# Performance work log

Hardware: AMD Instinct MI355X
Metric: run time of the kernel (lower is better)

The kernel has to match this reference:

```python
import jax, jax.numpy as jnp
import numpy as np

B, T, D = 16, 512, 256          # batch, seq_len, d_model (= num features = num graph nodes N)
H, MC, K, DE, DH = 4, 4, 3, 10, 128
GS, SS, AS = 4, 6, 4            # global/sector/asset regime states
TAU = 0.5
STEPS = 3                       # diffusion steps
HID = max(64, D)
DEC_H = max(64, D // 2)


def setup_inputs() -> dict:
    key = jax.random.key(0)
    ks = iter(jax.random.split(key, 64))

    def nrm(shape, s=0.02):
        return (s * jax.random.normal(next(ks), shape)).astype(jnp.float32)

    z = lambda *s: jnp.zeros(s, jnp.float32)
    o = lambda *s: jnp.ones(s, jnp.float32)
    p = dict(
        x=jax.random.normal(next(ks), (B, T, D), dtype=jnp.float32),
        # hierarchical regime controller
        gW1=nrm((D, HID)), gb1=z(HID), g_ln_w=o(HID), g_ln_b=z(HID),
        gW2=nrm((HID, GS)), gb2=z(GS),
        sW1=nrm((D, HID)), sb1=z(HID), sW2=nrm((HID, D * SS)), sb2=z(D * SS),
        aW1=nrm((D, HID)), ab1=z(HID), aW2=nrm((HID, D * AS)), ab2=z(D * AS),
        global_prior=z(GS), sector_prior=z(SS), asset_prior=z(AS),
        g2f=nrm((GS, D)),
        sector_emb=jax.random.normal(next(ks), (SS, D), dtype=jnp.float32),
        asset_emb=jax.random.normal(next(ks), (AS, D), dtype=jnp.float32),
        # bidirectional temporal scan (BI-Mamba stand-in)
        decay_f=nrm((D,), 1.0), decay_b=nrm((D,), 1.0),
        tW=nrm((D, D)), tb=z(D),
        # Bayesian MAGAC + diffusion graph prior
        psi=nrm((H, D, DE), 0.1), log_sigma=jnp.full((H,), -2.0, jnp.float32),
        step_logits=jnp.linspace(-1.0, 0.5, STEPS).astype(jnp.float32),
        noise_scale=jnp.full((STEPS,), 0.05, jnp.float32),
        Wk=nrm((K + 1, T, DH)),
        mean_w=nrm((DH,)), mean_b=z(), lv_w=nrm((DH,)), lv_b=z(),
        # risk-aware decoder
        dW1=nrm((D, DEC_H)), db1=z(DEC_H), d_ln_w=o(DEC_H), d_ln_b=z(DEC_H),
        mW=nrm((DEC_H,)), mb=z(), lvW=nrm((DEC_H,)), lvb=z(),
        cW=nrm((DEC_H,)), cb=z(),
    )
    return p


def _ln(h, w, b):
    m = h.mean(-1, keepdims=True)
    v = h.var(-1, keepdims=True)  # biased, matches torch LayerNorm
    return (h - m) / jnp.sqrt(v + 1e-5) * w + b


def _gelu(h):
    return jax.nn.gelu(h, approximate=False)


def _gumbel_softmax(k, logits):
    u = jax.random.uniform(k, logits.shape, minval=1e-6, maxval=1.0 - 1e-6)
    g = -jnp.log(-jnp.log(u))
    return jax.nn.softmax((logits + g) / TAU, axis=-1)


def _fwd(x, gW1, gb1, g_ln_w, g_ln_b, gW2, gb2, sW1, sb1, sW2, sb2,
         aW1, ab1, aW2, ab2, global_prior, sector_prior, asset_prior,
         g2f, sector_emb, asset_emb, decay_f, decay_b, tW, tb,
         psi, log_sigma, step_logits, noise_scale, Wk,
         mean_w, mean_b, lv_w, lv_b,
         dW1, db1, d_ln_w, d_ln_b, mW, mb, lvW, lvb, cW, cb):
    rk = jax.random.key(42)
    k_g, k_s, k_a, k_eps, k_diff = jax.random.split(rk, 5)

    # ---- hierarchical regime controller ----
    seq_mean = x.mean(1)                               # (B, D)
    diff_summary = (x[:, 1:] - x[:, :-1]).mean(1)      # (B, D)
    g_logits = _gelu(_ln(seq_mean @ gW1 + gb1, g_ln_w, g_ln_b)) @ gW2 + gb2
    s_logits = (_gelu(seq_mean @ sW1 + sb1) @ sW2 + sb2).reshape(B, D, SS)
    a_logits = (_gelu(diff_summary @ aW1 + ab1) @ aW2 + ab2).reshape(B, D, AS)
    g_probs = _gumbel_softmax(k_g, g_logits)
    s_probs = _gumbel_softmax(k_s, s_logits)
    a_probs = _gumbel_softmax(k_a, a_logits)
    global_gate = g_probs @ g2f                                   # (B, D)
    # diagonal of einsum('bfs,sd->bfd') == einsum('bfs,sf->bf')
    sector_gate = jnp.einsum('bfs,sf->bf', s_probs, sector_emb)
    asset_gate = jnp.einsum('bfs,sf->bf', a_probs, asset_emb)
    feature_gate = jax.nn.sigmoid(global_gate + sector_gate + asset_gate)
    gated_x = x * feature_gate[:, None, :]

    # ---- bidirectional temporal EMA scan (BI-Mamba stand-in) ----
    af = jax.nn.sigmoid(decay_f)
    abk = jax.nn.sigmoid(decay_b)
    xs = gated_x.transpose(1, 0, 2)                    # (T, B, D)

    def ema(a):
        def step(h, xt):
            h = a * h + (1.0 - a) * xt
            return h, h
        return step

    _, hf = jax.lax.scan(ema(af), jnp.zeros_like(xs[0]), xs)
    _, hb = jax.lax.scan(ema(abk), jnp.zeros_like(xs[0]), xs[::-1])
    temporal = (hf + hb[::-1]).transpose(1, 0, 2) @ tW + tb       # (B, T, D)
    node_major = temporal.transpose(0, 2, 1)                      # (B, N=D, T)

    # ---- Bayesian adjacency sampling (MC samples per head) ----
    logits = jnp.einsum('hne,hme->hnm', psi, psi) / jnp.sqrt(jnp.float32(DE))
    sigma = jnp.exp(log_sigma)                                    # (H,)
    eps = jax.random.normal(k_eps, (MC, H, D, D))
    A = jax.nn.softmax(logits[None] + sigma[None, :, None, None] * eps, axis=-1)

    # ---- diffusion refinement guided by regime features ----
    ctx = feature_gate.mean(0)
    ctx = ctx / (jnp.linalg.norm(ctx) + 1e-6)
    outer = ctx[:, None] * ctx[None, :]
    outer = outer / jnp.maximum(outer.sum(-1, keepdims=True), 1e-6)
    dkeys = jax.random.split(k_diff, STEPS)
    for s in range(STEPS):                             # fixed small loop, vectorized over (MC,H)
        alpha = jax.nn.sigmoid(step_logits[s])
        noise = noise_scale[s] * jax.random.normal(dkeys[s], A.shape)
        A = alpha * A + (1.0 - alpha) * outer + noise
        A = 0.5 * (A + jnp.swapaxes(A, -1, -2))
        A = jax.nn.softmax(A, axis=-1)

    # ---- K-hop graph conv, averaged over MC samples and heads ----
    Z = jnp.einsum('bnt,td->bnd', node_major, Wk[0])[None, None]  # hop 0
    P = jnp.broadcast_to(node_major, (MC, H, B, D, T))
    for k in range(1, K + 1):
        P = jnp.einsum('mhnp,mhbpt->mhbnt', A, P)
        Z = Z + jnp.einsum('mhbnt,td->mhbnd', P, Wk[k])
    Z = Z.mean((0, 1))                                            # (B, N, DH)
    graph_mean = Z @ mean_w + mean_b                              # (B, N)
    graph_logvar = Z @ lv_w + lv_b                                # (B, N)

    # ---- risk-aware decoder ----
    feat = _ln(_gelu(graph_mean @ dW1 + db1), d_ln_w, d_ln_b)     # (B, DEC_H)
    mean = feat @ mW + mb
    dec_logvar = feat @ lvW + lvb
    _cvar = jax.nn.sigmoid(feat @ cW + cb)  # auxiliary head (not in returned output)
    var = jnp.exp(dec_logvar) + jnp.exp(graph_logvar).sum(1)
    log_var = jnp.log(var)
    return jnp.stack([mean, log_var], axis=-1)                    # (B, 2)


def reference(x, gW1, gb1, g_ln_w, g_ln_b, gW2, gb2, sW1, sb1, sW2, sb2,
              aW1, ab1, aW2, ab2, global_prior, sector_prior, asset_prior,
              g2f, sector_emb, asset_emb, decay_f, decay_b, tW, tb,
              psi, log_sigma, step_logits, noise_scale, Wk,
              mean_w, mean_b, lv_w, lv_b,
              dW1, db1, d_ln_w, d_ln_b, mW, mb, lvW, lvb, cW, cb):
    return _fwd(x, gW1, gb1, g_ln_w, g_ln_b, gW2, gb2, sW1, sb1, sW2, sb2,
                aW1, ab1, aW2, ab2, global_prior, sector_prior, asset_prior,
                g2f, sector_emb, asset_emb, decay_f, decay_b, tW, tb,
                psi, log_sigma, step_logits, noise_scale, Wk,
                mean_w, mean_b, lv_w, lv_b,
                dW1, db1, d_ln_w, d_ln_b, mW, mb, lvW, lvb, cW, cb)
```

## Files before the change

kernel.cpp:

```cpp
#include <hip/hip_runtime.h>
#include <stdint.h>

#define PARTITIONABLE 1

namespace {

struct TFPair { uint32_t a, b; };

__host__ __device__ constexpr uint32_t rotl32(uint32_t x, int d) {
  return (x << d) | (x >> (32 - d));
}

__host__ __device__ constexpr TFPair tf2x32(uint32_t k0, uint32_t k1,
                                            uint32_t x0, uint32_t x1) {
  uint32_t k2 = k0 ^ k1 ^ 0x1BD11BDAu;
  x0 += k0; x1 += k1;
  x0 += x1; x1 = rotl32(x1, 13); x1 ^= x0;
  x0 += x1; x1 = rotl32(x1, 15); x1 ^= x0;
  x0 += x1; x1 = rotl32(x1, 26); x1 ^= x0;
  x0 += x1; x1 = rotl32(x1, 6);  x1 ^= x0;
  x0 += k1; x1 += k2 + 1u;
  x0 += x1; x1 = rotl32(x1, 17); x1 ^= x0;
  x0 += x1; x1 = rotl32(x1, 29); x1 ^= x0;
  x0 += x1; x1 = rotl32(x1, 16); x1 ^= x0;
  x0 += x1; x1 = rotl32(x1, 24); x1 ^= x0;
  x0 += k2; x1 += k0 + 2u;
  x0 += x1; x1 = rotl32(x1, 13); x1 ^= x0;
  x0 += x1; x1 = rotl32(x1, 15); x1 ^= x0;
  x0 += x1; x1 = rotl32(x1, 26); x1 ^= x0;
  x0 += x1; x1 = rotl32(x1, 6);  x1 ^= x0;
  x0 += k0; x1 += k1 + 3u;
  x0 += x1; x1 = rotl32(x1, 17); x1 ^= x0;
  x0 += x1; x1 = rotl32(x1, 29); x1 ^= x0;
  x0 += x1; x1 = rotl32(x1, 16); x1 ^= x0;
  x0 += x1; x1 = rotl32(x1, 24); x1 ^= x0;
  x0 += k1; x1 += k2 + 4u;
  x0 += x1; x1 = rotl32(x1, 13); x1 ^= x0;
  x0 += x1; x1 = rotl32(x1, 15); x1 ^= x0;
  x0 += x1; x1 = rotl32(x1, 26); x1 ^= x0;
  x0 += x1; x1 = rotl32(x1, 6);  x1 ^= x0;
  x0 += k2; x1 += k0 + 5u;
  return TFPair{x0, x1};
}

#if PARTITIONABLE
constexpr TFPair KG  = tf2x32(0u, 42u, 0u, 0u);
constexpr TFPair KS  = tf2x32(0u, 42u, 0u, 1u);
constexpr TFPair KA  = tf2x32(0u, 42u, 0u, 2u);
constexpr TFPair KE  = tf2x32(0u, 42u, 0u, 3u);
constexpr TFPair KD  = tf2x32(0u, 42u, 0u, 4u);
constexpr TFPair DK0 = tf2x32(KD.a, KD.b, 0u, 0u);
constexpr TFPair DK1 = tf2x32(KD.a, KD.b, 0u, 1u);
constexpr TFPair DK2 = tf2x32(KD.a, KD.b, 0u, 2u);
#else
constexpr TFPair SP0 = tf2x32(0u, 42u, 0u, 5u);
constexpr TFPair SP1 = tf2x32(0u, 42u, 1u, 6u);
constexpr TFPair SP2 = tf2x32(0u, 42u, 2u, 7u);
constexpr TFPair SP3 = tf2x32(0u, 42u, 3u, 8u);
constexpr TFPair SP4 = tf2x32(0u, 42u, 4u, 9u);
constexpr TFPair KG  = TFPair{SP0.a, SP1.a};
constexpr TFPair KS  = TFPair{SP2.a, SP3.a};
constexpr TFPair KA  = TFPair{SP4.a, SP0.b};
constexpr TFPair KE  = TFPair{SP1.b, SP2.b};
constexpr TFPair KD  = TFPair{SP3.b, SP4.b};
constexpr TFPair DP0 = tf2x32(KD.a, KD.b, 0u, 3u);
constexpr TFPair DP1 = tf2x32(KD.a, KD.b, 1u, 4u);
constexpr TFPair DP2 = tf2x32(KD.a, KD.b, 2u, 5u);
constexpr TFPair DK0 = TFPair{DP0.a, DP1.a};
constexpr TFPair DK1 = TFPair{DP2.a, DP0.b};
constexpr TFPair DK2 = TFPair{DP1.b, DP2.b};
#endif

__device__ __forceinline__ uint32_t rbits(uint32_t k0, uint32_t k1,
                                          uint32_t idx, uint32_t half) {
#if PARTITIONABLE
  TFPair t = tf2x32(k0, k1, 0u, idx);
  return t.a ^ t.b;
#else
  if (idx < half) return tf2x32(k0, k1, idx, idx + half).a;
  return tf2x32(k0, k1, idx - half, idx).b;
#endif
}

__device__ __forceinline__ float bits_to_u01(uint32_t bits) {
  return __uint_as_float((bits >> 9) | 0x3F800000u) - 1.0f;
}

__device__ __forceinline__ float gumbel_u(uint32_t k0, uint32_t k1,
                                          uint32_t idx, uint32_t half) {
  const float mn = 1e-6f;
  const float mx = 1.0f - 1e-6f;
  float f = bits_to_u01(rbits(k0, k1, idx, half));
  return fmaxf(mn, f * (mx - mn) + mn);
}

__device__ __forceinline__ float erfinv_f32(float x) {
  float w = -log1pf(-x * x);
  float p;
  if (w < 5.0f) {
    w -= 2.5f;
    p = 2.81022636e-08f;
    p = fmaf(p, w, 3.43273939e-07f);
    p = fmaf(p, w, -3.5233877e-06f);
    p = fmaf(p, w, -4.39150654e-06f);
    p = fmaf(p, w, 0.00021858087f);
    p = fmaf(p, w, -0.00125372503f);
    p = fmaf(p, w, -0.00417768164f);
    p = fmaf(p, w, 0.246640727f);
    p = fmaf(p, w, 1.50140941f);
  } else {
    w = sqrtf(w) - 3.0f;
    p = -0.000200214257f;
    p = fmaf(p, w, 0.000100950558f);
    p = fmaf(p, w, 0.00134934322f);
    p = fmaf(p, w, -0.00367342844f);
    p = fmaf(p, w, 0.00573950773f);
    p = fmaf(p, w, -0.0076224613f);
    p = fmaf(p, w, 0.00943887047f);
    p = fmaf(p, w, 1.00167406f);
    p = fmaf(p, w, 2.83297682f);
  }
  return p * x;
}

__device__ __forceinline__ float normal_from(uint32_t k0, uint32_t k1,
                                             uint32_t idx, uint32_t half) {
  const float lo = -0x1.fffffep-1f;
  float f = bits_to_u01(rbits(k0, k1, idx, half));
  float u = fmaxf(lo, f * 2.0f + lo);
  return 1.41421356237f * erfinv_f32(u);
}

__device__ __forceinline__ float gelu_f(float x) {
  return 0.5f * x * (1.0f + erff(x / 1.4142135623730951f));
}
__device__ __forceinline__ float sigmoid_f(float x) {
  return 1.0f / (1.0f + expf(-x));
}

__device__ __forceinline__ float wave_sum(float v) {
  #pragma unroll
  for (int m = 32; m > 0; m >>= 1) v += __shfl_xor(v, m);
  return v;
}
__device__ __forceinline__ float wave_max(float v) {
  #pragma unroll
  for (int m = 32; m > 0; m >>= 1) v = fmaxf(v, __shfl_xor(v, m));
  return v;
}
template <int NW>
__device__ __forceinline__ float blk_sum(float v, float* slots) {
  v = wave_sum(v);
  int wid = threadIdx.x >> 6;
  if ((threadIdx.x & 63) == 0) slots[wid] = v;
  __syncthreads();
  float r = slots[0];
  #pragma unroll
  for (int i = 1; i < NW; ++i) r += slots[i];
  return r;
}
template <int NW>
__device__ __forceinline__ float blk_max(float v, float* slots) {
  v = wave_max(v);
  int wid = threadIdx.x >> 6;
  if ((threadIdx.x & 63) == 0) slots[wid] = v;
  __syncthreads();
  float r = slots[0];
  #pragma unroll
  for (int i = 1; i < NW; ++i) r = fmaxf(r, slots[i]);
  return r;
}

struct Params {
  const float *x, *gW1, *gb1, *glnw, *glnb, *gW2, *gb2, *sW1, *sb1, *sW2, *sb2,
      *aW1, *ab1, *aW2, *ab2, *g2f, *semb, *aemb, *decay_f, *decay_b, *tW, *tb,
      *psi, *log_sigma, *step_logits, *noise_scale, *Wk, *mean_w, *mean_b,
      *lv_w, *lv_b, *dW1, *db1, *dlnw, *dlnb, *mW, *mb, *lvW, *lvb;
  float* out;
  float *ps, *ds, *hgG, *hgS, *hgA, *fg, *ctx, *v, *sv, *u, *Pf, *Qf, *Pb, *Qb,
      *Lf, *Lb, *YH, *R1, *R2, *gm, *glv, *A, *A2;
};


__device__ __forceinline__ void phase_hidden(const Params& P, float* smem,
                                             int bid, int tid) {
  float* inv = smem;
  float* s1 = smem + 256;
  float* s2 = smem + 260;
  int head = bid >> 4, b = bid & 15;
  float iv;
  if (head < 2) {
    float s = 0.f;
    for (int tc = 0; tc < 16; ++tc) s += P.ps[(size_t)(b * 16 + tc) * 256 + tid];
    iv = s / 512.0f;
  } else {
    iv = P.ds[b * 256 + tid];
  }
  inv[tid] = iv;
  __syncthreads();
  const float* W1 = (head == 0) ? P.gW1 : (head == 1) ? P.sW1 : P.aW1;
  const float* b1 = (head == 0) ? P.gb1 : (head == 1) ? P.sb1 : P.ab1;
  float h = b1[tid];
  for (int d = 0; d < 256; ++d) h = fmaf(inv[d], W1[d * 256 + tid], h);
  if (head == 0) {
    float mean = blk_sum<4>(h, s1) / 256.0f;
    float dv = h - mean;
    float var = blk_sum<4>(dv * dv, s2) / 256.0f;
    h = dv / sqrtf(var + 1e-5f) * P.glnw[tid] + P.glnb[tid];
  }
  float* outp = (head == 0) ? P.hgG : (head == 1) ? P.hgS : P.hgA;
  outp[b * 256 + tid] = gelu_f(h);
}

__device__ __forceinline__ void phase_vcompute(const Params& P, int bid2,
                                               int tid) {
  int j = bid2 >> 2, tg = bid2 & 3;
  const float* wp = (j & 1) ? P.lv_w : P.mean_w;
  const float* Wkk = P.Wk + (size_t)(j >> 1) * 65536;
  int wid = tid >> 6, lane = tid & 63;
  float w0 = wp[lane], w1 = wp[64 + lane];
  float svloc = 0.f;
  for (int i = 0; i < 32; ++i) {
    int t = tg * 128 + wid * 32 + i;
    const float* row = Wkk + (size_t)t * 128;
    float s = row[lane] * w0 + row[64 + lane] * w1;
    s = wave_sum(s);
    if (lane == 0) { P.v[j * 512 + t] = s; svloc += s; }
  }
  if (lane == 0) atomicAdd(&P.sv[j], svloc);
}

__device__ __forceinline__ void phase_ainit_row(const Params& P, float* smem,
                                                int blk, int tid) {
  float* pn = smem;
  float* s1 = smem + 12;
  float* s2 = smem + 16;
  int mh = blk >> 8, h = mh & 3, n = blk & 255, p = tid;
  if (p < 10) pn[p] = P.psi[(size_t)(h * 256 + n) * 10 + p];
  __syncthreads();
  const float* pp = P.psi + (size_t)(h * 256 + p) * 10;
  float s = 0.f;
  #pragma unroll
  for (int e = 0; e < 10; ++e) s = fmaf(pn[e], pp[e], s);
  float logit = s / sqrtf(10.0f);
  uint32_t idx = (uint32_t)blk * 256u + (uint32_t)p;
  float eps = normal_from(KE.a, KE.b, idx, 524288u);
  float val = logit + expf(P.log_sigma[h]) * eps;
  float mx = blk_max<4>(val, s1);
  float e = expf(val - mx);
  float sum = blk_sum<4>(e, s2);
  P.A[(size_t)blk * 256 + p] = e / sum;
}

__device__ __forceinline__ void phase_gates(const Params& P, float* smem,
                                            int bid, int tid) {
  float* hgGs = smem;
  float* hgSs = smem + 256;
  float* hgAs = smem + 512;
  float* lvS = smem + 768;
  float* lvA = smem + 1152;
  float* gsl = smem + 1408;
  float* gvals = smem + 1424;
  float* gpv = smem + 1428;
  int b = bid >> 2, f0 = (bid & 3) * 64;
  hgGs[tid] = P.hgG[b * 256 + tid];
  hgSs[tid] = P.hgS[b * 256 + tid];
  hgAs[tid] = P.hgA[b * 256 + tid];
  __syncthreads();
  float lg[4];
  #pragma unroll
  for (int s = 0; s < 4; ++s)
    lg[s] = blk_sum<4>(hgGs[tid] * P.gW2[tid * 4 + s], gsl + 4 * s);
  if (tid < 4) {
    float u = gumbel_u(KG.a, KG.b, (uint32_t)(b * 4 + tid), 32u);
    float g = -logf(-logf(u));
    gvals[tid] = (lg[tid] + P.gb2[tid] + g) / 0.5f;
  }
  __syncthreads();
  if (tid < 4) {
    float mx = fmaxf(fmaxf(gvals[0], gvals[1]), fmaxf(gvals[2], gvals[3]));
    float sum = expf(gvals[0] - mx) + expf(gvals[1] - mx) +
                expf(gvals[2] - mx) + expf(gvals[3] - mx);
    gpv[tid] = expf(gvals[tid] - mx) / sum;
  }
  {
    int o = tid;
    int fl = o / 6, s = o - fl * 6;
    int f = f0 + fl;
    const float* wp = P.sW2 + f * 6 + s;
    float acc = P.sb2[f * 6 + s];
    for (int d = 0; d < 256; ++d) acc = fmaf(hgSs[d], wp[(size_t)d * 1536], acc);
    float u = gumbel_u(KS.a, KS.b, (uint32_t)(b * 256 + f) * 6u + s, 12288u);
    lvS[o] = (acc + (-logf(-logf(u)))) / 0.5f;
  }
  if (tid < 128) {
    int o = tid + 256;
    int fl = o / 6, s = o - fl * 6;
    int f = f0 + fl;
    const float* wp = P.sW2 + f * 6 + s;
    float acc = P.sb2[f * 6 + s];
    for (int d = 0; d < 256; ++d) acc = fmaf(hgSs[d], wp[(size_t)d * 1536], acc);
    float u = gumbel_u(KS.a, KS.b, (uint32_t)(b * 256 + f) * 6u + s, 12288u);
    lvS[o] = (acc + (-logf(-logf(u)))) / 0.5f;
  }
  {
    int fl = tid >> 2, s = tid & 3;
    int f = f0 + fl;
    const float* wp = P.aW2 + f * 4 + s;
    float acc = P.ab2[f * 4 + s];
    for (int d = 0; d < 256; ++d) acc = fmaf(hgAs[d], wp[(size_t)d * 1024], acc);
    float u = gumbel_u(KA.a, KA.b, (uint32_t)(b * 256 + f) * 4u + s, 8192u);
    lvA[tid] = (acc + (-logf(-logf(u)))) / 0.5f;
  }
  __syncthreads();
  if (tid < 64) {
    int f = f0 + tid;
    float v0 = lvS[tid * 6 + 0], v1 = lvS[tid * 6 + 1], v2 = lvS[tid * 6 + 2];
    float v3 = lvS[tid * 6 + 3], v4 = lvS[tid * 6 + 4], v5 = lvS[tid * 6 + 5];
    float mx = fmaxf(fmaxf(fmaxf(v0, v1), fmaxf(v2, v3)), fmaxf(v4, v5));
    float e0 = expf(v0 - mx), e1 = expf(v1 - mx), e2 = expf(v2 - mx);
    float e3 = expf(v3 - mx), e4 = expf(v4 - mx), e5 = expf(v5 - mx);
    float ssum = e0 + e1 + e2 + e3 + e4 + e5;
    float sg = (e0 / ssum) * P.semb[0 * 256 + f] + (e1 / ssum) * P.semb[1 * 256 + f] +
               (e2 / ssum) * P.semb[2 * 256 + f] + (e3 / ssum) * P.semb[3 * 256 + f] +
               (e4 / ssum) * P.semb[4 * 256 + f] + (e5 / ssum) * P.semb[5 * 256 + f];
    float a0 = lvA[tid * 4 + 0], a1 = lvA[tid * 4 + 1];
    float a2 = lvA[tid * 4 + 2], a3 = lvA[tid * 4 + 3];
    float amx = fmaxf(fmaxf(a0, a1), fmaxf(a2, a3));
    float x0 = expf(a0 - amx), x1 = expf(a1 - amx);
    float x2 = expf(a2 - amx), x3 = expf(a3 - amx);
    float asum = x0 + x1 + x2 + x3;
    float ag = (x0 / asum) * P.aemb[0 * 256 + f] + (x1 / asum) * P.aemb[1 * 256 + f] +
               (x2 / asum) * P.aemb[2 * 256 + f] + (x3 / asum) * P.aemb[3 * 256 + f];
    float gg = 0.f;
    #pragma unroll
    for (int s = 0; s < 4; ++s) gg = fmaf(gpv[s], P.g2f[s * 256 + f], gg);
    P.fg[b * 256 + f] = sigmoid_f(gg + sg + ag);
  }
}

__device__ __forceinline__ void phase_ctx(const Params& P, float* smem,
                                          int tid) {
  float* s1 = smem;
  float* s2 = smem + 4;
  float c = 0.f;
  for (int b = 0; b < 16; ++b) c += P.fg[b * 256 + tid];
  c /= 16.0f;
  float ss = blk_sum<4>(c * c, s1);
  float cv = c / (sqrtf(ss) + 1e-6f);
  P.ctx[tid] = cv;
  float S = blk_sum<4>(cv, s2);
  if (tid == 0) P.ctx[256] = S;
}

__device__ __forceinline__ void phase_scan1(const Params& P, float* smem,
                                            int ch, int tid) {
  float* vv = smem;
  int b = ch >> 4, c = ch & 15;
  int d = tid;
  vv[(d >> 5) * 32 + (d & 31)] = P.v[(d >> 5) * 512 + c * 32 + (d & 31)];
  __syncthreads();
  float g = P.fg[b * 256 + d];
  float af = sigmoid_f(P.decay_f[d]);
  float ab = sigmoid_f(P.decay_b[d]);
  float r_gx[32];
  const float* xp = P.x + ((size_t)b * 512 + c * 32) * 256 + d;
  #pragma unroll
  for (int i = 0; i < 32; ++i) r_gx[i] = xp[(size_t)i * 256] * g;
  float h = 0.f, pw = 1.f;
  float Pr[8], Q[8];
  #pragma unroll
  for (int j = 0; j < 8; ++j) { Pr[j] = 0.f; Q[j] = 0.f; }
  #pragma unroll
  for (int i = 0; i < 32; ++i) {
    h = fmaf(af, h, (1.0f - af) * r_gx[i]);
    pw *= af;
    #pragma unroll
    for (int j = 0; j < 8; ++j) {
      float vj = vv[j * 32 + i];
      Pr[j] = fmaf(h, vj, Pr[j]);
      Q[j] = fmaf(pw, vj, Q[j]);
    }
  }
  size_t base = ((size_t)(b * 16 + c) * 8) * 256 + d;
  #pragma unroll
  for (int j = 0; j < 8; ++j) {
    P.Pf[base + j * 256] = Pr[j];
    P.Qf[base + j * 256] = Q[j];
  }
  P.Lf[(b * 16 + c) * 256 + d] = h;
  h = 0.f; pw = 1.f;
  #pragma unroll
  for (int j = 0; j < 8; ++j) { Pr[j] = 0.f; Q[j] = 0.f; }
  #pragma unroll
  for (int i = 31; i >= 0; --i) {
    h = fmaf(ab, h, (1.0f - ab) * r_gx[i]);
    pw *= ab;
    #pragma unroll
    for (int j = 0; j < 8; ++j) {
      float vj = vv[j * 32 + i];
      Pr[j] = fmaf(h, vj, Pr[j]);
      Q[j] = fmaf(pw, vj, Q[j]);
    }
  }
  #pragma unroll
  for (int j = 0; j < 8; ++j) {
    P.Pb[base + j * 256] = Pr[j];
    P.Qb[base + j * 256] = Q[j];
  }
  P.Lb[(b * 16 + c) * 256 + d] = h;
}

__device__ __forceinline__ void phase_scan2(const Params& P, int blk, int tid) {
  int b = blk >> 3, j = blk & 7;
  int d = tid;
  float af = sigmoid_f(P.decay_f[d]);
  float ab = sigmoid_f(P.decay_b[d]);
  float af32 = af, ab32 = ab;
  #pragma unroll
  for (int q = 0; q < 5; ++q) { af32 *= af32; ab32 *= ab32; }
  float acc = 0.f, H = 0.f;
  for (int c = 0; c < 16; ++c) {
    size_t base = ((size_t)(b * 16 + c) * 8 + j) * 256 + d;
    acc += P.Pf[base] + H * P.Qf[base];
    H = P.Lf[(b * 16 + c) * 256 + d] + af32 * H;
  }
  H = 0.f;
  for (int c = 15; c >= 0; --c) {
    size_t base = ((size_t)(b * 16 + c) * 8 + j) * 256 + d;
    acc += P.Pb[base] + H * P.Qb[base];
    H = P.Lb[(b * 16 + c) * 256 + d] + ab32 * H;
  }
  P.u[(b * 8 + j) * 256 + d] = acc;
}

__device__ __forceinline__ void phase_ygemm(const Params& P, float* smem,
                                            int blk32, int tid) {
  float* As = smem;
  float* Bs = smem + 1056;
  float* svs = smem + 2112;
  int n0 = (blk32 & 7) * 32, m0 = (blk32 >> 3) * 32;
  int tx = tid & 31, ty = tid >> 5;
  if (tid < 8) svs[tid] = P.sv[tid];
  float acc[4] = {0.f, 0.f, 0.f, 0.f};
  for (int k0 = 0; k0 < 256; k0 += 32) {
    #pragma unroll
    for (int l = 0; l < 4; ++l) {
      int e = tid + l * 256, r = e >> 5, cc = e & 31;
      As[r * 33 + cc] = P.u[(size_t)(m0 + r) * 256 + k0 + cc];
      Bs[r * 33 + cc] = P.tW[(size_t)(k0 + r) * 256 + n0 + cc];
    }
    __syncthreads();
    #pragma unroll
    for (int kk = 0; kk < 32; ++kk) {
      float bv = Bs[kk * 33 + tx];
      #pragma unroll
      for (int i = 0; i < 4; ++i)
        acc[i] = fmaf(As[(ty + 8 * i) * 33 + kk], bv, acc[i]);
    }
    __syncthreads();
  }
  int n = n0 + tx;
  float tbn = P.tb[n];
  float mb0 = P.mean_b[0], lb0 = P.lv_b[0];
  #pragma unroll
  for (int i = 0; i < 4; ++i) {
    int row = m0 + ty + 8 * i;
    int b = row >> 3, j = row & 7;
    float val = acc[i] + tbn * svs[j];
    if (j == 0) P.gm[b * 256 + n] = val + mb0;
    else if (j == 1) P.glv[b * 256 + n] = val + lb0;
    else {
      int k = (j >> 1) - 1, proj = j & 1;
      P.YH[k * 8192 + n * 32 + b * 2 + proj] = val;
    }
  }
}

__device__ __forceinline__ void phase_mix_row(const Params& P, float* smem,
                                              int sidx, const float* Ain,
                                              float* Aout, uint32_t dk0,
                                              uint32_t dk1, int blk, int tid) {
  float* s1 = smem;
  float* s2 = smem + 4;
  float alpha = sigmoid_f(P.step_logits[sidx]);
  float ns = P.noise_scale[sidx];
  float S = P.ctx[256];
  float cp = P.ctx[tid];
  int mh = blk >> 8, n = blk & 255, p = tid;
  float cn = P.ctx[n];
  float o_np = (cn * cp) / fmaxf(cn * S, 1e-6f);
  float o_pn = (cp * cn) / fmaxf(cp * S, 1e-6f);
  uint32_t i_np = (uint32_t)blk * 256u + (uint32_t)p;
  uint32_t i_pn = (uint32_t)mh * 65536u + (uint32_t)p * 256u + (uint32_t)n;
  float a_np = Ain[(size_t)mh * 65536 + n * 256 + p];
  float a_pn = Ain[(size_t)mh * 65536 + p * 256 + n];
  float m_np = alpha * a_np + (1.0f - alpha) * o_np +
               ns * normal_from(dk0, dk1, i_np, 524288u);
  float m_pn = alpha * a_pn + (1.0f - alpha) * o_pn +
               ns * normal_from(dk0, dk1, i_pn, 524288u);
  float val = 0.5f * (m_np + m_pn);
  float mx = blk_max<4>(val, s1);
  float e = expf(val - mx);
  float sum = blk_sum<4>(e, s2);
  Aout[(size_t)blk * 256 + p] = e / sum;
}

__device__ __forceinline__ void phase_horner(const Params& P, float* smem,
                                             const float* A, const float* Rin,
                                             int sRin, const float* Yadd,
                                             float* Rout, int bid, int tid) {
  float* As = smem;
  float* Bs = smem + 1056;
  int nt = bid & 7, mh = bid >> 3;
  int n0 = nt * 32;
  int tx = tid & 31, ty = tid >> 5;
  float acc[4] = {0.f, 0.f, 0.f, 0.f};
  const float* Ab = A + (size_t)mh * 65536;
  const float* Rb = Rin + (size_t)mh * sRin;
  for (int k0 = 0; k0 < 256; k0 += 32) {
    #pragma unroll
    for (int l = 0; l < 4; ++l) {
      int e = tid + l * 256, r = e >> 5, cc = e & 31;
      As[r * 33 + cc] = Ab[(size_t)(n0 + r) * 256 + k0 + cc];
      Bs[r * 33 + cc] = Rb[(size_t)(k0 + r) * 32 + cc];
    }
    __syncthreads();
    #pragma unroll
    for (int kk = 0; kk < 32; ++kk) {
      float bv = Bs[kk * 33 + tx];
      #pragma unroll
      for (int i = 0; i < 4; ++i)
        acc[i] = fmaf(As[(ty + 8 * i) * 33 + kk], bv, acc[i]);
    }
    __syncthreads();
  }
  #pragma unroll
  for (int i = 0; i < 4; ++i) {
    int n = n0 + ty + 8 * i;
    float vv = acc[i];
    if (Yadd) vv += Yadd[n * 32 + tx];
    Rout[(size_t)mh * 8192 + (size_t)n * 32 + tx] = vv;
  }
}

__device__ __forceinline__ void phase_findec(const Params& P, float* smem,
                                             int bid, int tid) {
  float* gmv = smem;
  float* sl = smem + 256;
  int b = bid;
  float sm_ = 0.f, sl_ = 0.f;
  for (int mh = 0; mh < 16; ++mh) {
    sm_ += P.R1[(size_t)mh * 8192 + tid * 32 + b * 2];
    sl_ += P.R1[(size_t)mh * 8192 + tid * 32 + b * 2 + 1];
  }
  float gmn = P.gm[b * 256 + tid] + sm_ * (1.0f / 16.0f);
  float gln = P.glv[b * 256 + tid] + sl_ * (1.0f / 16.0f);
  gmv[tid] = gmn;
  float se = expf(gln);
  __syncthreads();
  float sumexp = blk_sum<4>(se, sl);
  float h = 0.f;
  if (tid < 128) {
    h = P.db1[tid];
    for (int n = 0; n < 256; ++n) h = fmaf(gmv[n], P.dW1[n * 128 + tid], h);
    h = gelu_f(h);
  }
  float mean = blk_sum<4>(tid < 128 ? h : 0.f, sl + 4) / 128.0f;
  float dv = (tid < 128) ? h - mean : 0.f;
  float var = blk_sum<4>(dv * dv, sl + 8) / 128.0f;
  float feat = (tid < 128) ? dv / sqrtf(var + 1e-5f) * P.dlnw[tid] + P.dlnb[tid]
                           : 0.f;
  float m_c = blk_sum<4>(tid < 128 ? feat * P.mW[tid] : 0.f, sl + 12) + P.mb[0];
  float lv_c = blk_sum<4>(tid < 128 ? feat * P.lvW[tid] : 0.f, sl + 16) + P.lvb[0];
  if (tid == 0) {
    P.out[b * 2 + 0] = m_c;
    P.out[b * 2 + 1] = logf(expf(lv_c) + sumexp);
  }
}


__global__ __launch_bounds__(256) void kL0(Params P) {
  int bid = blockIdx.x, tid = threadIdx.x;
  int b = bid >> 4, tc = bid & 15;
  const float* xp = P.x + ((size_t)b * 512 + tc * 32) * 256 + tid;
  float s = 0.f;
  for (int i = 0; i < 32; ++i) s += xp[(size_t)i * 256];
  P.ps[(size_t)bid * 256 + tid] = s;
  if (tc == 0) {
    const float* xb = P.x + (size_t)b * 512 * 256 + tid;
    P.ds[b * 256 + tid] = (xb[(size_t)511 * 256] - xb[0]) / 511.0f;
  }
  if (bid == 0 && tid < 8) P.sv[tid] = 0.f;
}

__global__ __launch_bounds__(256) void kLA(Params P) {
  __shared__ float smem[20];
  phase_ainit_row(P, smem, blockIdx.x, threadIdx.x);
}

__global__ __launch_bounds__(256) void kLB(Params P) {
  __shared__ float smem[272];
  int bid = blockIdx.x, tid = threadIdx.x;
  if (bid < 48) phase_hidden(P, smem, bid, tid);
  else phase_vcompute(P, bid - 48, tid);
}

__global__ __launch_bounds__(256) void kLC(Params P) {
  __shared__ float smem[1440];
  phase_gates(P, smem, blockIdx.x, threadIdx.x);
}

__global__ __launch_bounds__(256) void kLD(Params P) {
  __shared__ float smem[256];
  int bid = blockIdx.x, tid = threadIdx.x;
  if (bid < 256) phase_scan1(P, smem, bid, tid);
  else phase_ctx(P, smem, tid);
}

__global__ __launch_bounds__(256) void kM0(Params P) {
  __shared__ float smem[8];
  int bid = blockIdx.x, tid = threadIdx.x;
  if (bid < 4096) phase_mix_row(P, smem, 0, P.A, P.A2, DK0.a, DK0.b, bid, tid);
  else phase_scan2(P, bid - 4096, tid);
}

__global__ __launch_bounds__(256) void kM1(Params P) {
  __shared__ float smem[2120];
  int bid = blockIdx.x, tid = threadIdx.x;
  if (bid < 4096) phase_mix_row(P, smem, 1, P.A2, P.A, DK1.a, DK1.b, bid, tid);
  else phase_ygemm(P, smem, bid - 4096, tid);
}

__global__ __launch_bounds__(256) void kM2(Params P) {
  __shared__ float smem[8];
  phase_mix_row(P, smem, 2, P.A, P.A2, DK2.a, DK2.b, blockIdx.x, threadIdx.x);
}

__global__ __launch_bounds__(256) void kH1(Params P) {
  __shared__ float smem[2112];
  phase_horner(P, smem, P.A2, P.YH + 2 * 8192, 0, P.YH + 8192, P.R1,
               blockIdx.x, threadIdx.x);
}
__global__ __launch_bounds__(256) void kH2(Params P) {
  __shared__ float smem[2112];
  phase_horner(P, smem, P.A2, P.R1, 8192, P.YH, P.R2, blockIdx.x, threadIdx.x);
}
__global__ __launch_bounds__(256) void kH3(Params P) {
  __shared__ float smem[2112];
  phase_horner(P, smem, P.A2, P.R2, 8192, nullptr, P.R1, blockIdx.x,
               threadIdx.x);
}

__global__ __launch_bounds__(256) void kFin(Params P) {
  __shared__ float smem[276];
  phase_findec(P, smem, blockIdx.x, threadIdx.x);
}

constexpr size_t O_PS = 0;
constexpr size_t O_DS = 65536;
constexpr size_t O_HGG = 69632;
constexpr size_t O_HGS = 73728;
constexpr size_t O_HGA = 77824;
constexpr size_t O_FG = 81920;
constexpr size_t O_CTX = 86016;
constexpr size_t O_V = 86336;
constexpr size_t O_SV = 90432;
constexpr size_t O_U = 90496;
constexpr size_t O_PF = 123264;
constexpr size_t O_QF = 647552;
constexpr size_t O_PB = 1171840;
constexpr size_t O_QB = 1696128;
constexpr size_t O_LF = 2220416;
constexpr size_t O_LB = 2285952;
constexpr size_t O_YH = 2351488;
constexpr size_t O_R1 = 2376064;
constexpr size_t O_R2 = 2507136;
constexpr size_t O_GM = 2638208;
constexpr size_t O_GLV = 2642304;
constexpr size_t O_A = 2646400;
constexpr size_t O_A2 = 3694976;

}

extern "C" void kernel_launch(void* const* d_in, const int* in_sizes, int n_in,
                              void* d_out, int out_size, void* d_ws,
                              size_t ws_size, hipStream_t stream) {
  (void)in_sizes; (void)n_in; (void)out_size; (void)ws_size;
  float* w = (float*)d_ws;
  Params prm;
  prm.x = (const float*)d_in[0];
  prm.gW1 = (const float*)d_in[1];
  prm.gb1 = (const float*)d_in[2];
  prm.glnw = (const float*)d_in[3];
  prm.glnb = (const float*)d_in[4];
  prm.gW2 = (const float*)d_in[5];
  prm.gb2 = (const float*)d_in[6];
  prm.sW1 = (const float*)d_in[7];
  prm.sb1 = (const float*)d_in[8];
  prm.sW2 = (const float*)d_in[9];
  prm.sb2 = (const float*)d_in[10];
  prm.aW1 = (const float*)d_in[11];
  prm.ab1 = (const float*)d_in[12];
  prm.aW2 = (const float*)d_in[13];
  prm.ab2 = (const float*)d_in[14];
  prm.g2f = (const float*)d_in[18];
  prm.semb = (const float*)d_in[19];
  prm.aemb = (const float*)d_in[20];
  prm.decay_f = (const float*)d_in[21];
  prm.decay_b = (const float*)d_in[22];
  prm.tW = (const float*)d_in[23];
  prm.tb = (const float*)d_in[24];
  prm.psi = (const float*)d_in[25];
  prm.log_sigma = (const float*)d_in[26];
  prm.step_logits = (const float*)d_in[27];
  prm.noise_scale = (const float*)d_in[28];
  prm.Wk = (const float*)d_in[29];
  prm.mean_w = (const float*)d_in[30];
  prm.mean_b = (const float*)d_in[31];
  prm.lv_w = (const float*)d_in[32];
  prm.lv_b = (const float*)d_in[33];
  prm.dW1 = (const float*)d_in[34];
  prm.db1 = (const float*)d_in[35];
  prm.dlnw = (const float*)d_in[36];
  prm.dlnb = (const float*)d_in[37];
  prm.mW = (const float*)d_in[38];
  prm.mb = (const float*)d_in[39];
  prm.lvW = (const float*)d_in[40];
  prm.lvb = (const float*)d_in[41];
  prm.out = (float*)d_out;
  prm.ps = w + O_PS;
  prm.ds = w + O_DS;
  prm.hgG = w + O_HGG;
  prm.hgS = w + O_HGS;
  prm.hgA = w + O_HGA;
  prm.fg = w + O_FG;
  prm.ctx = w + O_CTX;
  prm.v = w + O_V;
  prm.sv = w + O_SV;
  prm.u = w + O_U;
  prm.Pf = w + O_PF;
  prm.Qf = w + O_QF;
  prm.Pb = w + O_PB;
  prm.Qb = w + O_QB;
  prm.Lf = w + O_LF;
  prm.Lb = w + O_LB;
  prm.YH = w + O_YH;
  prm.R1 = w + O_R1;
  prm.R2 = w + O_R2;
  prm.gm = w + O_GM;
  prm.glv = w + O_GLV;
  prm.A = w + O_A;
  prm.A2 = w + O_A2;

  kL0<<<256, 256, 0, stream>>>(prm);
  kLA<<<4096, 256, 0, stream>>>(prm);
  kLB<<<80, 256, 0, stream>>>(prm);
  kLC<<<64, 256, 0, stream>>>(prm);
  kLD<<<257, 256, 0, stream>>>(prm);
  kM0<<<4224, 256, 0, stream>>>(prm);
  kM1<<<4128, 256, 0, stream>>>(prm);
  kM2<<<4096, 256, 0, stream>>>(prm);
  kH1<<<128, 256, 0, stream>>>(prm);
  kH2<<<128, 256, 0, stream>>>(prm);
  kH3<<<128, 256, 0, stream>>>(prm);
  kFin<<<16, 256, 0, stream>>>(prm);
}
```

Measured before the change: 316.7 us.

## Restructure pipeline: fuse prologue kernels, precompute diffusion noise, full serial scan

Merges the x-sum, attention init, noise generation and temporal scan into one large launch, and fuses the hidden layers with the gate computation. It moves the gate multiply out of the scan into the y-GEMM, which lets the scan be gate-independent and run in one pass per batch (serial over 512 steps) instead of as chunked partials plus a combine. Diffusion noise is precomputed into a workspace buffer rather than regenerated inside each mix step. The last Horner step now reduces straight into gm/glv with atomics. This cuts launches and intermediates, at the cost of a long serial scan on only 16 blocks and extra noise-buffer traffic. The scan blocks also recompute the Wk projection redundantly.

```diff
diff --git a/kernel.cpp b/kernel.cpp
--- a/kernel.cpp
+++ b/kernel.cpp
@@ -177,57 +177,20 @@
       *psi, *log_sigma, *step_logits, *noise_scale, *Wk, *mean_w, *mean_b,
       *lv_w, *lv_b, *dW1, *db1, *dlnw, *dlnb, *mW, *mb, *lvW, *lvb;
   float* out;
-  float *ps, *ds, *hgG, *hgS, *hgA, *fg, *ctx, *v, *sv, *u, *Pf, *Qf, *Pb, *Qb,
-      *Lf, *Lb, *YH, *R1, *R2, *gm, *glv, *A, *A2;
+  float *ps, *ds, *fg, *ctx, *sv, *u, *YH, *R1, *R2, *gm, *glv, *A, *A2, *nz;
 };
 
 
-__device__ __forceinline__ void phase_hidden(const Params& P, float* smem,
-                                             int bid, int tid) {
-  float* inv = smem;
-  float* s1 = smem + 256;
-  float* s2 = smem + 260;
-  int head = bid >> 4, b = bid & 15;
-  float iv;
-  if (head < 2) {
-    float s = 0.f;
-    for (int tc = 0; tc < 16; ++tc) s += P.ps[(size_t)(b * 16 + tc) * 256 + tid];
-    iv = s / 512.0f;
-  } else {
-    iv = P.ds[b * 256 + tid];
-  }
-  inv[tid] = iv;
-  __syncthreads();
-  const float* W1 = (head == 0) ? P.gW1 : (head == 1) ? P.sW1 : P.aW1;
-  const float* b1 = (head == 0) ? P.gb1 : (head == 1) ? P.sb1 : P.ab1;
-  float h = b1[tid];
-  for (int d = 0; d < 256; ++d) h = fmaf(inv[d], W1[d * 256 + tid], h);
-  if (head == 0) {
-    float mean = blk_sum<4>(h, s1) / 256.0f;
-    float dv = h - mean;
-    float var = blk_sum<4>(dv * dv, s2) / 256.0f;
-    h = dv / sqrtf(var + 1e-5f) * P.glnw[tid] + P.glnb[tid];
-  }
-  float* outp = (head == 0) ? P.hgG : (head == 1) ? P.hgS : P.hgA;
-  outp[b * 256 + tid] = gelu_f(h);
-}
-
-__device__ __forceinline__ void phase_vcompute(const Params& P, int bid2,
-                                               int tid) {
-  int j = bid2 >> 2, tg = bid2 & 3;
-  const float* wp = (j & 1) ? P.lv_w : P.mean_w;
-  const float* Wkk = P.Wk + (size_t)(j >> 1) * 65536;
-  int wid = tid >> 6, lane = tid & 63;
-  float w0 = wp[lane], w1 = wp[64 + lane];
-  float svloc = 0.f;
-  for (int i = 0; i < 32; ++i) {
-    int t = tg * 128 + wid * 32 + i;
-    const float* row = Wkk + (size_t)t * 128;
-    float s = row[lane] * w0 + row[64 + lane] * w1;
-    s = wave_sum(s);
-    if (lane == 0) { P.v[j * 512 + t] = s; svloc += s; }
-  }
-  if (lane == 0) atomicAdd(&P.sv[j], svloc);
+__device__ __forceinline__ void phase_xsum(const Params& P, int bid, int tid) {
+  int b = bid >> 4, tc = bid & 15;
+  const float* xp = P.x + ((size_t)b * 512 + tc * 32) * 256 + tid;
+  float s = 0.f;
+  for (int i = 0; i < 32; ++i) s += xp[(size_t)i * 256];
+  P.ps[(size_t)bid * 256 + tid] = s;
+  if (tc == 0) {
+    const float* xb = P.x + (size_t)b * 512 * 256 + tid;
+    P.ds[b * 256 + tid] = (xb[(size_t)511 * 256] - xb[0]) / 511.0f;
+  }
 }
 
 __device__ __forceinline__ void phase_ainit_row(const Params& P, float* smem,
@@ -252,25 +215,102 @@
   P.A[(size_t)blk * 256 + p] = e / sum;
 }
 
-__device__ __forceinline__ void phase_gates(const Params& P, float* smem,
-                                            int bid, int tid) {
-  float* hgGs = smem;
-  float* hgSs = smem + 256;
-  float* hgAs = smem + 512;
-  float* lvS = smem + 768;
-  float* lvA = smem + 1152;
-  float* gsl = smem + 1408;
-  float* gvals = smem + 1424;
-  float* gpv = smem + 1428;
+__device__ __forceinline__ void phase_noise(const Params& P, int blk2,
+                                            int tid) {
+  const uint32_t dka[3] = {DK0.a, DK1.a, DK2.a};
+  const uint32_t dkb[3] = {DK0.b, DK1.b, DK2.b};
+  int s = blk2 >> 12;
+  int row = blk2 & 4095;
+  uint32_t e = (uint32_t)row * 256u + (uint32_t)tid;
+  float z = normal_from(dka[s], dkb[s], e, 524288u);
+  P.nz[(size_t)s * 1048576 + e] = P.noise_scale[s] * z;
+}
+
+__device__ __forceinline__ void phase_fullscan(const Params& P, float* vsh,
+                                               int b, int tid) {
+  for (int jt = tid; jt < 4096; jt += 256) {
+    int j = jt >> 9, t = jt & 511;
+    const float* row = P.Wk + (size_t)(j >> 1) * 65536 + (size_t)t * 128;
+    const float* wp = (j & 1) ? P.lv_w : P.mean_w;
+    float s = 0.f;
+    for (int e = 0; e < 128; ++e) s = fmaf(row[e], wp[e], s);
+    vsh[j * 512 + t] = s;
+  }
+  __syncthreads();
+  if (b == 0 && tid < 8) {
+    float s = 0.f;
+    for (int t = 0; t < 512; ++t) s += vsh[tid * 512 + t];
+    P.sv[tid] = s;
+  }
+  int d = tid;
+  float af = sigmoid_f(P.decay_f[d]);
+  float ab = sigmoid_f(P.decay_b[d]);
+  const float* xb = P.x + (size_t)b * 512 * 256 + d;
+  float acc[8];
+  #pragma unroll
+  for (int j = 0; j < 8; ++j) acc[j] = 0.f;
+  float h = 0.f;
+  for (int t = 0; t < 512; ++t) {
+    float xv = xb[(size_t)t * 256];
+    h = fmaf(af, h, (1.0f - af) * xv);
+    #pragma unroll
+    for (int j = 0; j < 8; ++j) acc[j] = fmaf(h, vsh[j * 512 + t], acc[j]);
+  }
+  h = 0.f;
+  for (int t = 511; t >= 0; --t) {
+    float xv = xb[(size_t)t * 256];
+    h = fmaf(ab, h, (1.0f - ab) * xv);
+    #pragma unroll
+    for (int j = 0; j < 8; ++j) acc[j] = fmaf(h, vsh[j * 512 + t], acc[j]);
+  }
+  #pragma unroll
+  for (int j = 0; j < 8; ++j) P.u[(size_t)(b * 8 + j) * 256 + d] = acc[j];
+}
+
+__device__ __forceinline__ void phase_hidden_gates(const Params& P,
+                                                   float* smem, int bid,
+                                                   int tid) {
+  float* sms = smem;
+  float* dss = smem + 256;
+  float* hgG = smem + 512;
+  float* hgS = smem + 768;
+  float* hgA = smem + 1024;
+  float* lvS = smem + 1280;
+  float* lvA = smem + 1664;
+  float* gsl = smem + 1920;
+  float* gvals = smem + 1936;
+  float* gpv = smem + 1940;
+  float* s1 = smem + 1944;
+  float* s2 = smem + 1948;
   int b = bid >> 2, f0 = (bid & 3) * 64;
-  hgGs[tid] = P.hgG[b * 256 + tid];
-  hgSs[tid] = P.hgS[b * 256 + tid];
-  hgAs[tid] = P.hgA[b * 256 + tid];
+  {
+    float s = 0.f;
+    for (int tc = 0; tc < 16; ++tc)
+      s += P.ps[(size_t)(b * 16 + tc) * 256 + tid];
+    sms[tid] = s / 512.0f;
+    dss[tid] = P.ds[b * 256 + tid];
+  }
+  __syncthreads();
+  {
+    float h = P.gb1[tid];
+    for (int d = 0; d < 256; ++d) h = fmaf(sms[d], P.gW1[d * 256 + tid], h);
+    float mean = blk_sum<4>(h, s1) / 256.0f;
+    float dv = h - mean;
+    float var = blk_sum<4>(dv * dv, s2) / 256.0f;
+    h = dv / sqrtf(var + 1e-5f) * P.glnw[tid] + P.glnb[tid];
+    hgG[tid] = gelu_f(h);
+    float h2 = P.sb1[tid];
+    for (int d = 0; d < 256; ++d) h2 = fmaf(sms[d], P.sW1[d * 256 + tid], h2);
+    hgS[tid] = gelu_f(h2);
+    float h3 = P.ab1[tid];
+    for (int d = 0; d < 256; ++d) h3 = fmaf(dss[d], P.aW1[d * 256 + tid], h3);
+    hgA[tid] = gelu_f(h3);
+  }
   __syncthreads();
   float lg[4];
   #pragma unroll
   for (int s = 0; s < 4; ++s)
-    lg[s] = blk_sum<4>(hgGs[tid] * P.gW2[tid * 4 + s], gsl + 4 * s);
+    lg[s] = blk_sum<4>(hgG[tid] * P.gW2[tid * 4 + s], gsl + 4 * s);
   if (tid < 4) {
     float u = gumbel_u(KG.a, KG.b, (uint32_t)(b * 4 + tid), 32u);
     float g = -logf(-logf(u));
@@ -289,7 +329,7 @@
     int f = f0 + fl;
     const float* wp = P.sW2 + f * 6 + s;
     float acc = P.sb2[f * 6 + s];
-    for (int d = 0; d < 256; ++d) acc = fmaf(hgSs[d], wp[(size_t)d * 1536], acc);
+    for (int d = 0; d < 256; ++d) acc = fmaf(hgS[d], wp[(size_t)d * 1536], acc);
     float u = gumbel_u(KS.a, KS.b, (uint32_t)(b * 256 + f) * 6u + s, 12288u);
     lvS[o] = (acc + (-logf(-logf(u)))) / 0.5f;
   }
@@ -299,7 +339,7 @@
     int f = f0 + fl;
     const float* wp = P.sW2 + f * 6 + s;
     float acc = P.sb2[f * 6 + s];
-    for (int d = 0; d < 256; ++d) acc = fmaf(hgSs[d], wp[(size_t)d * 1536], acc);
+    for (int d = 0; d < 256; ++d) acc = fmaf(hgS[d], wp[(size_t)d * 1536], acc);
     float u = gumbel_u(KS.a, KS.b, (uint32_t)(b * 256 + f) * 6u + s, 12288u);
     lvS[o] = (acc + (-logf(-logf(u)))) / 0.5f;
   }
@@ -308,7 +348,7 @@
     int f = f0 + fl;
     const float* wp = P.aW2 + f * 4 + s;
     float acc = P.ab2[f * 4 + s];
-    for (int d = 0; d < 256; ++d) acc = fmaf(hgAs[d], wp[(size_t)d * 1024], acc);
+    for (int d = 0; d < 256; ++d) acc = fmaf(hgA[d], wp[(size_t)d * 1024], acc);
     float u = gumbel_u(KA.a, KA.b, (uint32_t)(b * 256 + f) * 4u + s, 8192u);
     lvA[tid] = (acc + (-logf(-logf(u)))) / 0.5f;
   }
@@ -353,87 +393,6 @@
   if (tid == 0) P.ctx[256] = S;
 }
 
-__device__ __forceinline__ void phase_scan1(const Params& P, float* smem,
-                                            int ch, int tid) {
-  float* vv = smem;
-  int b = ch >> 4, c = ch & 15;
-  int d = tid;
-  vv[(d >> 5) * 32 + (d & 31)] = P.v[(d >> 5) * 512 + c * 32 + (d & 31)];
-  __syncthreads();
-  float g = P.fg[b * 256 + d];
-  float af = sigmoid_f(P.decay_f[d]);
-  float ab = sigmoid_f(P.decay_b[d]);
-  float r_gx[32];
-  const float* xp = P.x + ((size_t)b * 512 + c * 32) * 256 + d;
-  #pragma unroll
-  for (int i = 0; i < 32; ++i) r_gx[i] = xp[(size_t)i * 256] * g;
-  float h = 0.f, pw = 1.f;
-  float Pr[8], Q[8];
-  #pragma unroll
-  for (int j = 0; j < 8; ++j) { Pr[j] = 0.f; Q[j] = 0.f; }
-  #pragma unroll
-  for (int i = 0; i < 32; ++i) {
-    h = fmaf(af, h, (1.0f - af) * r_gx[i]);
-    pw *= af;
-    #pragma unroll
-    for (int j = 0; j < 8; ++j) {
-      float vj = vv[j * 32 + i];
-      Pr[j] = fmaf(h, vj, Pr[j]);
-      Q[j] = fmaf(pw, vj, Q[j]);
-    }
-  }
-  size_t base = ((size_t)(b * 16 + c) * 8) * 256 + d;
-  #pragma unroll
-  for (int j = 0; j < 8; ++j) {
-    P.Pf[base + j * 256] = Pr[j];
-    P.Qf[base + j * 256] = Q[j];
-  }
-  P.Lf[(b * 16 + c) * 256 + d] = h;
-  h = 0.f; pw = 1.f;
-  #pragma unroll
-  for (int j = 0; j < 8; ++j) { Pr[j] = 0.f; Q[j] = 0.f; }
-  #pragma unroll
-  for (int i = 31; i >= 0; --i) {
-    h = fmaf(ab, h, (1.0f - ab) * r_gx[i]);
-    pw *= ab;
-    #pragma unroll
-    for (int j = 0; j < 8; ++j) {
-      float vj = vv[j * 32 + i];
-      Pr[j] = fmaf(h, vj, Pr[j]);
-      Q[j] = fmaf(pw, vj, Q[j]);
-    }
-  }
-  #pragma unroll
-  for (int j = 0; j < 8; ++j) {
-    P.Pb[base + j * 256] = Pr[j];
-    P.Qb[base + j * 256] = Q[j];
-  }
-  P.Lb[(b * 16 + c) * 256 + d] = h;
-}
-
-__device__ __forceinline__ void phase_scan2(const Params& P, int blk, int tid) {
-  int b = blk >> 3, j = blk & 7;
-  int d = tid;
-  float af = sigmoid_f(P.decay_f[d]);
-  float ab = sigmoid_f(P.decay_b[d]);
-  float af32 = af, ab32 = ab;
-  #pragma unroll
-  for (int q = 0; q < 5; ++q) { af32 *= af32; ab32 *= ab32; }
-  float acc = 0.f, H = 0.f;
-  for (int c = 0; c < 16; ++c) {
-    size_t base = ((size_t)(b * 16 + c) * 8 + j) * 256 + d;
-    acc += P.Pf[base] + H * P.Qf[base];
-    H = P.Lf[(b * 16 + c) * 256 + d] + af32 * H;
-  }
-  H = 0.f;
-  for (int c = 15; c >= 0; --c) {
-    size_t base = ((size_t)(b * 16 + c) * 8 + j) * 256 + d;
-    acc += P.Pb[base] + H * P.Qb[base];
-    H = P.Lb[(b * 16 + c) * 256 + d] + ab32 * H;
-  }
-  P.u[(b * 8 + j) * 256 + d] = acc;
-}
-
 __device__ __forceinline__ void phase_ygemm(const Params& P, float* smem,
                                             int blk32, int tid) {
   float* As = smem;
@@ -447,7 +406,9 @@
     #pragma unroll
     for (int l = 0; l < 4; ++l) {
       int e = tid + l * 256, r = e >> 5, cc = e & 31;
-      As[r * 33 + cc] = P.u[(size_t)(m0 + r) * 256 + k0 + cc];
+      int row = m0 + r;
+      As[r * 33 + cc] = P.u[(size_t)row * 256 + k0 + cc] *
+                        P.fg[(row >> 3) * 256 + k0 + cc];
       Bs[r * 33 + cc] = P.tW[(size_t)(k0 + r) * 256 + n0 + cc];
     }
     __syncthreads();
@@ -479,26 +440,23 @@
 
 __device__ __forceinline__ void phase_mix_row(const Params& P, float* smem,
                                               int sidx, const float* Ain,
-                                              float* Aout, uint32_t dk0,
-                                              uint32_t dk1, int blk, int tid) {
+                                              float* Aout, int blk, int tid) {
   float* s1 = smem;
   float* s2 = smem + 4;
   float alpha = sigmoid_f(P.step_logits[sidx]);
-  float ns = P.noise_scale[sidx];
   float S = P.ctx[256];
   float cp = P.ctx[tid];
   int mh = blk >> 8, n = blk & 255, p = tid;
   float cn = P.ctx[n];
   float o_np = (cn * cp) / fmaxf(cn * S, 1e-6f);
   float o_pn = (cp * cn) / fmaxf(cp * S, 1e-6f);
-  uint32_t i_np = (uint32_t)blk * 256u + (uint32_t)p;
-  uint32_t i_pn = (uint32_t)mh * 65536u + (uint32_t)p * 256u + (uint32_t)n;
+  const float* nzs = P.nz + (size_t)sidx * 1048576;
+  float nz_np = nzs[(size_t)blk * 256 + p];
+  float nz_pn = nzs[(size_t)mh * 65536 + (size_t)p * 256 + n];
   float a_np = Ain[(size_t)mh * 65536 + n * 256 + p];
   float a_pn = Ain[(size_t)mh * 65536 + p * 256 + n];
-  float m_np = alpha * a_np + (1.0f - alpha) * o_np +
-               ns * normal_from(dk0, dk1, i_np, 524288u);
-  float m_pn = alpha * a_pn + (1.0f - alpha) * o_pn +
-               ns * normal_from(dk0, dk1, i_pn, 524288u);
+  float m_np = alpha * a_np + (1.0f - alpha) * o_np + nz_np;
+  float m_pn = alpha * a_pn + (1.0f - alpha) * o_pn + nz_pn;
   float val = 0.5f * (m_np + m_pn);
   float mx = blk_max<4>(val, s1);
   float e = expf(val - mx);
@@ -544,18 +502,50 @@
   }
 }
 
+__device__ __forceinline__ void phase_horner_final(const Params& P,
+                                                   float* smem, int bid,
+                                                   int tid) {
+  float* As = smem;
+  float* Bs = smem + 1056;
+  int nt = bid & 7, mh = bid >> 3;
+  int n0 = nt * 32;
+  int tx = tid & 31, ty = tid >> 5;
+  float acc[4] = {0.f, 0.f, 0.f, 0.f};
+  const float* Ab = P.A2 + (size_t)mh * 65536;
+  const float* Rb = P.R2 + (size_t)mh * 8192;
+  for (int k0 = 0; k0 < 256; k0 += 32) {
+    #pragma unroll
+    for (int l = 0; l < 4; ++l) {
+      int e = tid + l * 256, r = e >> 5, cc = e & 31;
+      As[r * 33 + cc] = Ab[(size_t)(n0 + r) * 256 + k0 + cc];
+      Bs[r * 33 + cc] = Rb[(size_t)(k0 + r) * 32 + cc];
+    }
+    __syncthreads();
+    #pragma unroll
+    for (int kk = 0; kk < 32; ++kk) {
+      float bv = Bs[kk * 33 + tx];
+      #pragma unroll
+      for (int i = 0; i < 4; ++i)
+        acc[i] = fmaf(As[(ty + 8 * i) * 33 + kk], bv, acc[i]);
+    }
+    __syncthreads();
+  }
+  int bb = tx >> 1, proj = tx & 1;
+  float* dst = proj ? P.glv : P.gm;
+  #pragma unroll
+  for (int i = 0; i < 4; ++i) {
+    int n = n0 + ty + 8 * i;
+    atomicAdd(dst + bb * 256 + n, acc[i] * 0.0625f);
+  }
+}
+
 __device__ __forceinline__ void phase_findec(const Params& P, float* smem,
                                              int bid, int tid) {
   float* gmv = smem;
   float* sl = smem + 256;
   int b = bid;
-  float sm_ = 0.f, sl_ = 0.f;
-  for (int mh = 0; mh < 16; ++mh) {
-    sm_ += P.R1[(size_t)mh * 8192 + tid * 32 + b * 2];
-    sl_ += P.R1[(size_t)mh * 8192 + tid * 32 + b * 2 + 1];
-  }
-  float gmn = P.gm[b * 256 + tid] + sm_ * (1.0f / 16.0f);
-  float gln = P.glv[b * 256 + tid] + sl_ * (1.0f / 16.0f);
+  float gmn = P.gm[b * 256 + tid];
+  float gln = P.glv[b * 256 + tid];
   gmv[tid] = gmn;
   float se = expf(gln);
   __syncthreads();
@@ -580,61 +570,38 @@
 }
 
 
-__global__ __launch_bounds__(256) void kL0(Params P) {
+__global__ __launch_bounds__(256) void kN0(Params P) {
+  __shared__ float smem[4096];
   int bid = blockIdx.x, tid = threadIdx.x;
-  int b = bid >> 4, tc = bid & 15;
-  const float* xp = P.x + ((size_t)b * 512 + tc * 32) * 256 + tid;
-  float s = 0.f;
-  for (int i = 0; i < 32; ++i) s += xp[(size_t)i * 256];
-  P.ps[(size_t)bid * 256 + tid] = s;
-  if (tc == 0) {
-    const float* xb = P.x + (size_t)b * 512 * 256 + tid;
-    P.ds[b * 256 + tid] = (xb[(size_t)511 * 256] - xb[0]) / 511.0f;
-  }
-  if (bid == 0 && tid < 8) P.sv[tid] = 0.f;
-}
-
-__global__ __launch_bounds__(256) void kLA(Params P) {
-  __shared__ float smem[20];
-  phase_ainit_row(P, smem, blockIdx.x, threadIdx.x);
-}
-
-__global__ __launch_bounds__(256) void kLB(Params P) {
-  __shared__ float smem[272];
+  if (bid < 256) phase_xsum(P, bid, tid);
+  else if (bid < 4352) phase_ainit_row(P, smem, bid - 256, tid);
+  else if (bid < 16640) phase_noise(P, bid - 4352, tid);
+  else phase_fullscan(P, smem, bid - 16640, tid);
+}
+
+__global__ __launch_bounds__(256) void kN1(Params P) {
+  __shared__ float smem[1952];
+  phase_hidden_gates(P, smem, blockIdx.x, threadIdx.x);
+}
+
+__global__ __launch_bounds__(256) void kN2(Params P) {
+  __shared__ float smem[2120];
   int bid = blockIdx.x, tid = threadIdx.x;
-  if (bid < 48) phase_hidden(P, smem, bid, tid);
-  else phase_vcompute(P, bid - 48, tid);
-}
-
-__global__ __launch_bounds__(256) void kLC(Params P) {
-  __shared__ float smem[1440];
-  phase_gates(P, smem, blockIdx.x, threadIdx.x);
-}
-
-__global__ __launch_bounds__(256) void kLD(Params P) {
-  __shared__ float smem[256];
-  int bid = blockIdx.x, tid = threadIdx.x;
-  if (bid < 256) phase_scan1(P, smem, bid, tid);
+  if (bid < 32) phase_ygemm(P, smem, bid, tid);
   else phase_ctx(P, smem, tid);
 }
 
 __global__ __launch_bounds__(256) void kM0(Params P) {
   __shared__ float smem[8];
-  int bid = blockIdx.x, tid = threadIdx.x;
-  if (bid < 4096) phase_mix_row(P, smem, 0, P.A, P.A2, DK0.a, DK0.b, bid, tid);
-  else phase_scan2(P, bid - 4096, tid);
-}
-
+  phase_mix_row(P, smem, 0, P.A, P.A2, blockIdx.x, threadIdx.x);
+}
 __global__ __launch_bounds__(256) void kM1(Params P) {
-  __shared__ float smem[2120];
-  int bid = blockIdx.x, tid = threadIdx.x;
-  if (bid < 4096) phase_mix_row(P, smem, 1, P.A2, P.A, DK1.a, DK1.b, bid, tid);
-  else phase_ygemm(P, smem, bid - 4096, tid);
-}
-
+  __shared__ float smem[8];
+  phase_mix_row(P, smem, 1, P.A2, P.A, blockIdx.x, threadIdx.x);
+}
 __global__ __launch_bounds__(256) void kM2(Params P) {
   __shared__ float smem[8];
-  phase_mix_row(P, smem, 2, P.A, P.A2, DK2.a, DK2.b, blockIdx.x, threadIdx.x);
+  phase_mix_row(P, smem, 2, P.A, P.A2, blockIdx.x, threadIdx.x);
 }
 
 __global__ __launch_bounds__(256) void kH1(Params P) {
@@ -648,8 +615,7 @@
 }
 __global__ __launch_bounds__(256) void kH3(Params P) {
   __shared__ float smem[2112];
-  phase_horner(P, smem, P.A2, P.R2, 8192, nullptr, P.R1, blockIdx.x,
-               threadIdx.x);
+  phase_horner_final(P, smem, blockIdx.x, threadIdx.x);
 }
 
 __global__ __launch_bounds__(256) void kFin(Params P) {
@@ -659,27 +625,18 @@
 
 constexpr size_t O_PS = 0;
 constexpr size_t O_DS = 65536;
-constexpr size_t O_HGG = 69632;
-constexpr size_t O_HGS = 73728;
-constexpr size_t O_HGA = 77824;
-constexpr size_t O_FG = 81920;
-constexpr size_t O_CTX = 86016;
-constexpr size_t O_V = 86336;
-constexpr size_t O_SV = 90432;
-constexpr size_t O_U = 90496;
-constexpr size_t O_PF = 123264;
-constexpr size_t O_QF = 647552;
-constexpr size_t O_PB = 1171840;
-constexpr size_t O_QB = 1696128;
-constexpr size_t O_LF = 2220416;
-constexpr size_t O_LB = 2285952;
-constexpr size_t O_YH = 2351488;
-constexpr size_t O_R1 = 2376064;
-constexpr size_t O_R2 = 2507136;
-constexpr size_t O_GM = 2638208;
-constexpr size_t O_GLV = 2642304;
-constexpr size_t O_A = 2646400;
-constexpr size_t O_A2 = 3694976;
+constexpr size_t O_FG = 69632;
+constexpr size_t O_CTX = 73728;
+constexpr size_t O_SV = 74048;
+constexpr size_t O_U = 74112;
+constexpr size_t O_YH = 106880;
+constexpr size_t O_R1 = 131456;
+constexpr size_t O_R2 = 262528;
+constexpr size_t O_GM = 393600;
+constexpr size_t O_GLV = 397696;
+constexpr size_t O_A = 401792;
+constexpr size_t O_A2 = 1450368;
+constexpr size_t O_NZ = 2498944;
 
 }
 
@@ -731,20 +688,10 @@
   prm.out = (float*)d_out;
   prm.ps = w + O_PS;
   prm.ds = w + O_DS;
-  prm.hgG = w + O_HGG;
-  prm.hgS = w + O_HGS;
-  prm.hgA = w + O_HGA;
   prm.fg = w + O_FG;
   prm.ctx = w + O_CTX;
-  prm.v = w + O_V;
   prm.sv = w + O_SV;
   prm.u = w + O_U;
-  prm.Pf = w + O_PF;
-  prm.Qf = w + O_QF;
-  prm.Pb = w + O_PB;
-  prm.Qb = w + O_QB;
-  prm.Lf = w + O_LF;
-  prm.Lb = w + O_LB;
   prm.YH = w + O_YH;
   prm.R1 = w + O_R1;
   prm.R2 = w + O_R2;
@@ -752,14 +699,13 @@
   prm.glv = w + O_GLV;
   prm.A = w + O_A;
   prm.A2 = w + O_A2;
-
-  kL0<<<256, 256, 0, stream>>>(prm);
-  kLA<<<4096, 256, 0, stream>>>(prm);
-  kLB<<<80, 256, 0, stream>>>(prm);
-  kLC<<<64, 256, 0, stream>>>(prm);
-  kLD<<<257, 256, 0, stream>>>(prm);
-  kM0<<<4224, 256, 0, stream>>>(prm);
-  kM1<<<4128, 256, 0, stream>>>(prm);
+  prm.nz = w + O_NZ;
+
+  kN0<<<16656, 256, 0, stream>>>(prm);
+  kN1<<<64, 256, 0, stream>>>(prm);
+  kN2<<<33, 256, 0, stream>>>(prm);
+  kM0<<<4096, 256, 0, stream>>>(prm);
+  kM1<<<4096, 256, 0, stream>>>(prm);
   kM2<<<4096, 256, 0, stream>>>(prm);
   kH1<<<128, 256, 0, stream>>>(prm);
   kH2<<<128, 256, 0, stream>>>(prm);
```

After: 464.3 us. 1.47x slower.
